# Performance work log

Measured on AMD Instinct MI355X. Metric: run time of the kernel, lower is better.

Reference implementation:

```python
import jax, jax.numpy as jnp
import numpy as np

N = 50000
E = 800000
D = 128
EPS = 1e-5


def _init_lin(key, d_in, d_out):
    return (jax.random.normal(key, (d_out, d_in), dtype=jnp.float32) / np.sqrt(d_in)).astype(jnp.float32)


def setup_inputs() -> dict:
    key = jax.random.key(0)
    ks = jax.random.split(key, 16)
    x = jax.random.normal(ks[0], (N, D), dtype=jnp.float32)
    edge_index = jax.random.randint(ks[1], (2, E), 0, N, dtype=jnp.int32)
    inp = {"x": x, "edge_index": edge_index}
    # 3 SAGEConv layers: Wl (neighbor/aggr path, with bias), Wr (root path, no bias)
    for i in range(3):
        inp[f"Wl{i}"] = _init_lin(ks[2 + 3 * i], D, D)
        inp[f"bl{i}"] = jnp.zeros((D,), dtype=jnp.float32)
        inp[f"Wr{i}"] = _init_lin(ks[3 + 3 * i], D, D)
    # single LayerNorm (applied after conv0 only, since len(norms)=num_layers-2=1)
    inp["ln_g"] = jnp.ones((D,), dtype=jnp.float32)
    inp["ln_b"] = jnp.zeros((D,), dtype=jnp.float32)
    return inp


def _sage_conv(x, src, dst, Wl, bl, Wr):
    # sum-aggregate source features into destination nodes: [N, D]
    agg = jax.ops.segment_sum(x[src], dst, num_segments=N)
    return agg @ Wl.T + bl + x @ Wr.T


def _layernorm(h, g, b):
    mu = jnp.mean(h, axis=-1, keepdims=True)
    var = jnp.mean(jnp.square(h - mu), axis=-1, keepdims=True)
    return (h - mu) * jax.lax.rsqrt(var + EPS) * g + b


def reference(x, edge_index, Wl0, bl0, Wr0, Wl1, bl1, Wr1, Wl2, bl2, Wr2, ln_g, ln_b):
    src, dst = edge_index[0], edge_index[1]
    # layer 0: conv -> layernorm -> relu (dropout inactive in eval)
    h = _sage_conv(x, src, dst, Wl0, bl0, Wr0)
    h = jax.nn.relu(_layernorm(h, ln_g, ln_b))
    # layer 1: conv -> relu (no norm: i >= len(norms))
    h = jax.nn.relu(_sage_conv(h, src, dst, Wl1, bl1, Wr1))
    # layer 2: final conv, no activation
    return _sage_conv(h, src, dst, Wl2, bl2, Wr2)
```

## Files before the change

### kernel.cpp

```cpp
#include <hip/hip_runtime.h>
#include <hip/hip_bf16.h>

#define NN 50000
#define EE 800000
#define DD 128
#define SLOTS 64
#define GEMM_BLOCKS 782
#define PLACE_THREADS (GEMM_BLOCKS * 256)

typedef __attribute__((ext_vector_type(8))) short short8;
typedef __attribute__((ext_vector_type(4))) float floatx4;
typedef __attribute__((ext_vector_type(4))) unsigned short ushort4_t;

__device__ __forceinline__ short f2bf(float f) {
  union { float f; unsigned u; } c; c.f = f;
  unsigned r = c.u + 0x7FFFu + ((c.u >> 16) & 1u);
  return (short)(r >> 16);
}
__device__ __forceinline__ float bf2f(short s) {
  union { unsigned u; float f; } c; c.u = ((unsigned)(unsigned short)s) << 16;
  return c.f;
}
__device__ __forceinline__ unsigned pk(float a, float b) {
  return ((unsigned)(unsigned short)f2bf(a)) | (((unsigned)(unsigned short)f2bf(b)) << 16);
}

__global__ __launch_bounds__(256) void init_k(
    int* __restrict__ fill, int* __restrict__ Udummy,
    const float* __restrict__ W0, const float* __restrict__ W1,
    const float* __restrict__ W2, const float* __restrict__ W3,
    const float* __restrict__ W4, const float* __restrict__ W5,
    short* __restrict__ Wbf) {
  int i = blockIdx.x * 256 + threadIdx.x;
  if (i < NN) fill[i] = 0;
  if (i < 64) Udummy[i] = 0;
  int mat = i >> 14, local = i & 16383;
  const float* W;
  switch (mat) {
    case 0: W = W0; break;
    case 1: W = W1; break;
    case 2: W = W2; break;
    case 3: W = W3; break;
    case 4: W = W4; break;
    default: W = W5; break;
  }
  int r = local >> 7, c = local & 127;
  int idx = r * DD + (((c >> 3) ^ (r & 15)) << 3) + (c & 7);
  Wbf[(mat << 14) + idx] = f2bf(W[local]);
}

template <int BF16IN, int VBF16, int PLACE>
__global__ __launch_bounds__(256) void dual_gemm(
    const void* __restrict__ Ain, const short* __restrict__ Wpair,
    const float* __restrict__ bias,
    short* __restrict__ U, void* __restrict__ V,
    const int* __restrict__ srcE, const int* __restrict__ dstE,
    int* __restrict__ fill, unsigned short* __restrict__ srcSorted)
{
  __shared__ __align__(16) short lw[2 * DD * DD];
  int t = threadIdx.x;
  {
    const short8* gp = (const short8*)Wpair;
    short8* lp = (short8*)lw;
#pragma unroll
    for (int i = 0; i < 16; ++i) lp[t + i * 256] = gp[t + i * 256];
  }

  int wave = t >> 6, lane = t & 63;
  int m = lane & 15, q = lane >> 4;
  int node = blockIdx.x * 64 + wave * 16 + m;
  int ar = node < NN ? node : NN - 1;

  short8 af[4];
  if (BF16IN) {
    const short* H = (const short*)Ain + (size_t)ar * DD;
#pragma unroll
    for (int kc = 0; kc < 4; ++kc) af[kc] = *(const short8*)(H + kc * 32 + q * 8);
  } else {
    const floatx4* ap = (const floatx4*)((const float*)Ain + (size_t)ar * DD);
#pragma unroll
    for (int kc = 0; kc < 4; ++kc) {
      floatx4 p0 = ap[kc * 8 + q * 2];
      floatx4 p1 = ap[kc * 8 + q * 2 + 1];
      short8 s;
      s[0] = f2bf(p0[0]); s[1] = f2bf(p0[1]); s[2] = f2bf(p0[2]); s[3] = f2bf(p0[3]);
      s[4] = f2bf(p1[0]); s[5] = f2bf(p1[1]); s[6] = f2bf(p1[2]); s[7] = f2bf(p1[3]);
      af[kc] = s;
    }
  }
  __syncthreads();

  bool ok = node < NN;
#pragma unroll
  for (int ct = 0; ct < 8; ++ct) {
    floatx4 au = {0.f, 0.f, 0.f, 0.f}, av = {0.f, 0.f, 0.f, 0.f};
    int colq = ct * 16 + q * 4;
    const short* pl = &lw[(ct * 16 + m) * DD];
    const short* pr = &lw[DD * DD + (ct * 16 + m) * DD];
#pragma unroll
    for (int kc = 0; kc < 4; ++kc) {
      int pos = (((kc * 4 + q) ^ m) << 3);
      short8 bl_ = *(const short8*)(pl + pos);
      short8 br_ = *(const short8*)(pr + pos);
      au = __builtin_amdgcn_mfma_f32_16x16x32_bf16(bl_, af[kc], au, 0, 0, 0);
      av = __builtin_amdgcn_mfma_f32_16x16x32_bf16(br_, af[kc], av, 0, 0, 0);
    }
    if (ok) {
      uint2 uv;
      uv.x = pk(au[0], au[1]);
      uv.y = pk(au[2], au[3]);
      *(uint2*)(U + (size_t)node * DD + colq) = uv;
      floatx4 bv = *(const floatx4*)(bias + colq);
      if (VBF16) {
        uint2 vv;
        vv.x = pk(av[0] + bv[0], av[1] + bv[1]);
        vv.y = pk(av[2] + bv[2], av[3] + bv[3]);
        *(uint2*)((short*)V + (size_t)node * DD + colq) = vv;
      } else {
        floatx4 vv = {av[0] + bv[0], av[1] + bv[1], av[2] + bv[2], av[3] + bv[3]};
        *(floatx4*)((float*)V + (size_t)node * DD + colq) = vv;
      }
    }
  }

  if (PLACE) {
    int tid = blockIdx.x * 256 + t;
#pragma unroll
    for (int k = 0; k < 4; ++k) {
      int e = tid + k * PLACE_THREADS;
      if (e < EE) {
        int d = dstE[e];
        int slot = atomicAdd(&fill[d], 1);
        if (slot < SLOTS) srcSorted[(size_t)d * SLOTS + slot] = (unsigned short)srcE[e];
      }
    }
  }
}

template <int MODE>
__global__ __launch_bounds__(256) void agg_fuse(
    const short* __restrict__ U, const unsigned short* __restrict__ srcSorted,
    const int* __restrict__ fill, const short* __restrict__ Vbf,
    float* __restrict__ Vf, short* __restrict__ H,
    const float* __restrict__ g, const float* __restrict__ b)
{
  int node = blockIdx.x * 4 + (threadIdx.x >> 6);
  int lane = threadIdx.x & 63;
  int c = lane & 15, r = lane >> 4;
  int coff = c << 3;

  int deg = fill[node];
  deg = deg < SLOTS ? deg : SLOTS;
  const unsigned short* seg = srcSorted + (size_t)node * SLOTS;

  float acc[8] = {0.f, 0.f, 0.f, 0.f, 0.f, 0.f, 0.f, 0.f};
  int nbatch = (deg + 15) >> 4;
  for (int bb = 0; bb < nbatch; ++bb) {
    int s0 = bb * 16 + (r << 2);
    ushort4_t idx = *(const ushort4_t*)(seg + s0);
    int ra0 = (s0 + 0) < deg ? (int)idx[0] : NN;
    int ra1 = (s0 + 1) < deg ? (int)idx[1] : NN;
    int ra2 = (s0 + 2) < deg ? (int)idx[2] : NN;
    int ra3 = (s0 + 3) < deg ? (int)idx[3] : NN;
    short8 v0 = *(const short8*)(U + ((size_t)ra0 << 7) + coff);
    short8 v1 = *(const short8*)(U + ((size_t)ra1 << 7) + coff);
    short8 v2 = *(const short8*)(U + ((size_t)ra2 << 7) + coff);
    short8 v3 = *(const short8*)(U + ((size_t)ra3 << 7) + coff);
#pragma unroll
    for (int j = 0; j < 8; ++j)
      acc[j] += (bf2f(v0[j]) + bf2f(v1[j])) + (bf2f(v2[j]) + bf2f(v3[j]));
  }
#pragma unroll
  for (int j = 0; j < 8; ++j) {
    acc[j] += __shfl_xor(acc[j], 16, 64);
    acc[j] += __shfl_xor(acc[j], 32, 64);
  }

  if (MODE == 0) {
    short8 vv = *(const short8*)(Vbf + ((size_t)node << 7) + coff);
#pragma unroll
    for (int j = 0; j < 8; ++j) acc[j] += bf2f(vv[j]);
    float s = 0.f;
#pragma unroll
    for (int j = 0; j < 8; ++j) s += acc[j];
    s += __shfl_xor(s, 1, 64); s += __shfl_xor(s, 2, 64);
    s += __shfl_xor(s, 4, 64); s += __shfl_xor(s, 8, 64);
    float mu = s * (1.0f / 128.0f);
    float q2 = 0.f;
#pragma unroll
    for (int j = 0; j < 8; ++j) { float d = acc[j] - mu; q2 += d * d; }
    q2 += __shfl_xor(q2, 1, 64); q2 += __shfl_xor(q2, 2, 64);
    q2 += __shfl_xor(q2, 4, 64); q2 += __shfl_xor(q2, 8, 64);
    float rstd = rsqrtf(q2 * (1.0f / 128.0f) + 1e-5f);
    floatx4 g0 = *(const floatx4*)(g + coff), g1 = *(const floatx4*)(g + coff + 4);
    floatx4 b0 = *(const floatx4*)(b + coff), b1 = *(const floatx4*)(b + coff + 4);
    float o[8];
#pragma unroll
    for (int j = 0; j < 4; ++j) {
      o[j]     = (acc[j]     - mu) * rstd * g0[j] + b0[j];
      o[4 + j] = (acc[4 + j] - mu) * rstd * g1[j] + b1[j];
    }
#pragma unroll
    for (int j = 0; j < 8; ++j) o[j] = o[j] > 0.f ? o[j] : 0.f;
    if (r == 0) {
      uint4 pkt = {pk(o[0], o[1]), pk(o[2], o[3]), pk(o[4], o[5]), pk(o[6], o[7])};
      *(uint4*)(H + ((size_t)node << 7) + coff) = pkt;
    }
  } else if (MODE == 1) {
    if (r == 0) {
      short8 vv = *(const short8*)(Vbf + ((size_t)node << 7) + coff);
#pragma unroll
      for (int j = 0; j < 8; ++j) {
        acc[j] += bf2f(vv[j]);
        acc[j] = acc[j] > 0.f ? acc[j] : 0.f;
      }
      uint4 pkt = {pk(acc[0], acc[1]), pk(acc[2], acc[3]),
                   pk(acc[4], acc[5]), pk(acc[6], acc[7])};
      *(uint4*)(H + ((size_t)node << 7) + coff) = pkt;
    }
  } else {
    if (r == 0) {
      float* vp = Vf + ((size_t)node << 7) + coff;
      floatx4 a0 = ((const floatx4*)vp)[0];
      floatx4 a1 = ((const floatx4*)vp)[1];
      floatx4 o0 = {acc[0] + a0[0], acc[1] + a0[1], acc[2] + a0[2], acc[3] + a0[3]};
      floatx4 o1 = {acc[4] + a1[0], acc[5] + a1[1], acc[6] + a1[2], acc[7] + a1[3]};
      ((floatx4*)vp)[0] = o0;
      ((floatx4*)vp)[1] = o1;
    }
  }
}

extern "C" void kernel_launch(void* const* d_in, const int* in_sizes, int n_in,
                              void* d_out, int out_size, void* d_ws, size_t ws_size,
                              hipStream_t stream) {
  const float* x   = (const float*)d_in[0];
  const int*   ei  = (const int*)d_in[1];
  const int* src = ei;
  const int* dst = ei + EE;
  const float* Wl0 = (const float*)d_in[2];
  const float* bl0 = (const float*)d_in[3];
  const float* Wr0 = (const float*)d_in[4];
  const float* Wl1 = (const float*)d_in[5];
  const float* bl1 = (const float*)d_in[6];
  const float* Wr1 = (const float*)d_in[7];
  const float* Wl2 = (const float*)d_in[8];
  const float* bl2 = (const float*)d_in[9];
  const float* Wr2 = (const float*)d_in[10];
  const float* lng = (const float*)d_in[11];
  const float* lnb = (const float*)d_in[12];

  short* Vbf = (short*)d_out;
  float* Vf  = (float*)d_out;

  short* U   = (short*)d_ws;
  short* Hb  = U + (size_t)(NN + 1) * DD;
  short* Wbf = Hb + (size_t)NN * DD;
  unsigned short* srcS = (unsigned short*)(Wbf + 6 * DD * DD);
  int* fill  = (int*)(srcS + (size_t)NN * SLOTS);

  dim3 blk(256);

  init_k<<<384, blk, 0, stream>>>(fill, (int*)(U + (size_t)NN * DD),
                                  Wl0, Wr0, Wl1, Wr1, Wl2, Wr2, Wbf);

  dual_gemm<0, 1, 1><<<GEMM_BLOCKS, blk, 0, stream>>>(
      x, Wbf + 0 * 2 * DD * DD, bl0, U, Vbf, src, dst, fill, srcS);
  agg_fuse<0><<<NN / 4, blk, 0, stream>>>(U, srcS, fill, Vbf, Vf, Hb, lng, lnb);

  dual_gemm<1, 1, 0><<<GEMM_BLOCKS, blk, 0, stream>>>(
      Hb, Wbf + 1 * 2 * DD * DD, bl1, U, Vbf, src, dst, fill, srcS);
  agg_fuse<1><<<NN / 4, blk, 0, stream>>>(U, srcS, fill, Vbf, Vf, Hb, lng, lnb);

  dual_gemm<1, 0, 0><<<GEMM_BLOCKS, blk, 0, stream>>>(
      Hb, Wbf + 2 * 2 * DD * DD, bl2, U, Vf, src, dst, fill, srcS);
  agg_fuse<2><<<NN / 4, blk, 0, stream>>>(U, srcS, fill, Vbf, Vf, Hb, lng, lnb);
}
```

Measured before the change: 291.6 us.

## Split edge placement into partitioned kernel and stage GEMM outputs through LDS

Moves the edge-bucketing atomics out of the first GEMM into a separate place_k kernel. That kernel partitions destinations by d&7 so each block group handles one eighth of the nodes, and the fill counters are remapped to a partitioned layout to localise atomics. The dual GEMM now stages its U/V results in swizzled shared memory and writes them out as fully coalesced rows instead of scattered 8-byte fragments. This adds an extra kernel launch, makes every edge be read 8 times in place_k, and adds register pressure from holding all accumulators.

```diff
diff --git a/kernel.cpp b/kernel.cpp
--- a/kernel.cpp
+++ b/kernel.cpp
@@ -5,8 +5,8 @@
 #define EE 800000
 #define DD 128
 #define SLOTS 64
+#define PART 6250
 #define GEMM_BLOCKS 782
-#define PLACE_THREADS (GEMM_BLOCKS * 256)
 
 typedef __attribute__((ext_vector_type(8))) short short8;
 typedef __attribute__((ext_vector_type(4))) float floatx4;
@@ -49,13 +49,28 @@
   Wbf[(mat << 14) + idx] = f2bf(W[local]);
 }
 
-template <int BF16IN, int VBF16, int PLACE>
+__global__ __launch_bounds__(256) void place_k(
+    const int* __restrict__ srcE, const int* __restrict__ dstE,
+    int* __restrict__ fill, unsigned short* __restrict__ srcSorted) {
+  int p = blockIdx.x & 7;
+  int stripe = blockIdx.x >> 3;
+  int base = stripe * (EE / 64);
+  for (int i = threadIdx.x; i < EE / 64; i += 256) {
+    int e = base + i;
+    int d = dstE[e];
+    int s = srcE[e];
+    if ((d & 7) == p) {
+      int slot = atomicAdd(&fill[p * PART + (d >> 3)], 1);
+      if (slot < SLOTS) srcSorted[(size_t)d * SLOTS + slot] = (unsigned short)s;
+    }
+  }
+}
+
+template <int BF16IN, int VBF16>
 __global__ __launch_bounds__(256) void dual_gemm(
     const void* __restrict__ Ain, const short* __restrict__ Wpair,
     const float* __restrict__ bias,
-    short* __restrict__ U, void* __restrict__ V,
-    const int* __restrict__ srcE, const int* __restrict__ dstE,
-    int* __restrict__ fill, unsigned short* __restrict__ srcSorted)
+    short* __restrict__ U, void* __restrict__ V)
 {
   __shared__ __align__(16) short lw[2 * DD * DD];
   int t = threadIdx.x;
@@ -90,7 +105,9 @@
   }
   __syncthreads();
 
-  bool ok = node < NN;
+  uint2 uacc[8];
+  uint2 vaccb[8];
+  floatx4 vaccf[8];
 #pragma unroll
   for (int ct = 0; ct < 8; ++ct) {
     floatx4 au = {0.f, 0.f, 0.f, 0.f}, av = {0.f, 0.f, 0.f, 0.f};
@@ -105,33 +122,61 @@
       au = __builtin_amdgcn_mfma_f32_16x16x32_bf16(bl_, af[kc], au, 0, 0, 0);
       av = __builtin_amdgcn_mfma_f32_16x16x32_bf16(br_, af[kc], av, 0, 0, 0);
     }
-    if (ok) {
-      uint2 uv;
-      uv.x = pk(au[0], au[1]);
-      uv.y = pk(au[2], au[3]);
-      *(uint2*)(U + (size_t)node * DD + colq) = uv;
-      floatx4 bv = *(const floatx4*)(bias + colq);
+    floatx4 bv = *(const floatx4*)(bias + colq);
+    uacc[ct].x = pk(au[0], au[1]);
+    uacc[ct].y = pk(au[2], au[3]);
+    if (VBF16) {
+      vaccb[ct].x = pk(av[0] + bv[0], av[1] + bv[1]);
+      vaccb[ct].y = pk(av[2] + bv[2], av[3] + bv[3]);
+    } else {
+      floatx4 vv = {av[0] + bv[0], av[1] + bv[1], av[2] + bv[2], av[3] + bv[3]};
+      vaccf[ct] = vv;
+    }
+  }
+  __syncthreads();
+
+  {
+    int lrow = wave * 16 + m;
+    short* su = lw;
+#pragma unroll
+    for (int ct = 0; ct < 8; ++ct) {
+      int p = (ct * 4 + q) ^ m;
+      *(uint2*)(su + lrow * 128 + p * 4) = uacc[ct];
+    }
+    if (VBF16) {
+      short* sv = lw + 8192;
+#pragma unroll
+      for (int ct = 0; ct < 8; ++ct) {
+        int p = (ct * 4 + q) ^ m;
+        *(uint2*)(sv + lrow * 128 + p * 4) = vaccb[ct];
+      }
+    } else {
+      float* sv = (float*)(lw + 8192);
+#pragma unroll
+      for (int ct = 0; ct < 8; ++ct) {
+        int p = (ct * 4 + q) ^ m;
+        *(floatx4*)(sv + lrow * 128 + p * 4) = vaccf[ct];
+      }
+    }
+  }
+  __syncthreads();
+
+  int base = blockIdx.x * 64;
+#pragma unroll
+  for (int it = 0; it < 8; ++it) {
+    int f = it * 256 + t;
+    int row = f >> 5, gi = f & 31;
+    int nd = base + row;
+    if (nd < NN) {
+      int p = gi ^ (row & 15);
+      uint2 u = *(const uint2*)(lw + row * 128 + p * 4);
+      *(uint2*)(U + (size_t)nd * DD + gi * 4) = u;
       if (VBF16) {
-        uint2 vv;
-        vv.x = pk(av[0] + bv[0], av[1] + bv[1]);
-        vv.y = pk(av[2] + bv[2], av[3] + bv[3]);
-        *(uint2*)((short*)V + (size_t)node * DD + colq) = vv;
+        uint2 v = *(const uint2*)(lw + 8192 + row * 128 + p * 4);
+        *(uint2*)((short*)V + (size_t)nd * DD + gi * 4) = v;
       } else {
-        floatx4 vv = {av[0] + bv[0], av[1] + bv[1], av[2] + bv[2], av[3] + bv[3]};
-        *(floatx4*)((float*)V + (size_t)node * DD + colq) = vv;
-      }
-    }
-  }
-
-  if (PLACE) {
-    int tid = blockIdx.x * 256 + t;
-#pragma unroll
-    for (int k = 0; k < 4; ++k) {
-      int e = tid + k * PLACE_THREADS;
-      if (e < EE) {
-        int d = dstE[e];
-        int slot = atomicAdd(&fill[d], 1);
-        if (slot < SLOTS) srcSorted[(size_t)d * SLOTS + slot] = (unsigned short)srcE[e];
+        floatx4 v = *(const floatx4*)((const float*)(lw + 8192) + row * 128 + p * 4);
+        *(floatx4*)((float*)V + (size_t)nd * DD + gi * 4) = v;
       }
     }
   }
@@ -149,7 +194,7 @@
   int c = lane & 15, r = lane >> 4;
   int coff = c << 3;
 
-  int deg = fill[node];
+  int deg = fill[(node & 7) * PART + (node >> 3)];
   deg = deg < SLOTS ? deg : SLOTS;
   const unsigned short* seg = srcSorted + (size_t)node * SLOTS;
 
@@ -263,16 +308,17 @@
 
   init_k<<<384, blk, 0, stream>>>(fill, (int*)(U + (size_t)NN * DD),
                                   Wl0, Wr0, Wl1, Wr1, Wl2, Wr2, Wbf);
-
-  dual_gemm<0, 1, 1><<<GEMM_BLOCKS, blk, 0, stream>>>(
-      x, Wbf + 0 * 2 * DD * DD, bl0, U, Vbf, src, dst, fill, srcS);
+  place_k<<<512, blk, 0, stream>>>(src, dst, fill, srcS);
+
+  dual_gemm<0, 1><<<GEMM_BLOCKS, blk, 0, stream>>>(
+      x, Wbf + 0 * 2 * DD * DD, bl0, U, Vbf);
   agg_fuse<0><<<NN / 4, blk, 0, stream>>>(U, srcS, fill, Vbf, Vf, Hb, lng, lnb);
 
-  dual_gemm<1, 1, 0><<<GEMM_BLOCKS, blk, 0, stream>>>(
-      Hb, Wbf + 1 * 2 * DD * DD, bl1, U, Vbf, src, dst, fill, srcS);
+  dual_gemm<1, 1><<<GEMM_BLOCKS, blk, 0, stream>>>(
+      Hb, Wbf + 1 * 2 * DD * DD, bl1, U, Vbf);
   agg_fuse<1><<<NN / 4, blk, 0, stream>>>(U, srcS, fill, Vbf, Vf, Hb, lng, lnb);
 
-  dual_gemm<1, 0, 0><<<GEMM_BLOCKS, blk, 0, stream>>>(
-      Hb, Wbf + 2 * 2 * DD * DD, bl2, U, Vf, src, dst, fill, srcS);
+  dual_gemm<1, 0><<<GEMM_BLOCKS, blk, 0, stream>>>(
+      Hb, Wbf + 2 * 2 * DD * DD, bl2, U, Vf);
   agg_fuse<2><<<NN / 4, blk, 0, stream>>>(U, srcS, fill, Vbf, Vf, Hb, lng, lnb);
 }
```

Measured after the change: 279.0 us. -4.3%, faster.
